# Kernel optimization log

Hardware: AMD Instinct MI355X
Metric: run time of the kernel (lower is better)

Reference implementation:

```python
import jax, jax.numpy as jnp
import numpy as np
from jax import lax

DN = ('NCHW', 'OIHW', 'NCHW')


def setup_inputs() -> dict:
    key = jax.random.key(0)
    ks = jax.random.split(key, 7)
    B, IC, OC, H, W = 8, 64, 64, 128, 128
    return {
        'x': jax.random.normal(ks[0], (B, IC, H, W), jnp.float32),
        'w3': jax.random.normal(ks[1], (OC, IC, 3, 3), jnp.float32) * 0.05,
        'b3': jax.random.normal(ks[2], (OC,), jnp.float32) * 0.05,
        'w5': jax.random.normal(ks[3], (OC, IC, 5, 5), jnp.float32) * 0.05,
        'b5': jax.random.normal(ks[4], (OC,), jnp.float32) * 0.05,
        'wr': jax.random.normal(ks[5], (OC, 10, 1, 1), jnp.float32) * 0.1,
        'br': jax.random.normal(ks[6], (OC,), jnp.float32) * 0.05,
    }


def reference(x, w3, b3, w5, b5, wr, br):
    # Two 'same' convs (k=3 pad 1, k=5 pad 2) as in layers['5']
    y3 = lax.conv_general_dilated(x, w3, (1, 1), 'SAME', dimension_numbers=DN) + b3[None, :, None, None]
    y5 = lax.conv_general_dilated(x, w5, (1, 1), 'SAME', dimension_numbers=DN) + b5[None, :, None, None]
    B, C, H, W = y3.shape
    # The nested pad/crop loop == 9 zero-padded unit shifts of y3:
    # stackedFeatures order per channel: [y5, shift(sh=0,sw=0..2), shift(sh=1,...), ...]
    # shifted[h, w] = y3[h + 1 - sw, w + 1 - sh] with zero padding.
    P = jnp.pad(y3, ((0, 0), (0, 0), (1, 1), (1, 1)))
    shifts = [P[:, :, 2 - sw:2 - sw + H, 2 - sh:2 - sh + W]
              for sh in range(3) for sw in range(3)]
    stacked = jnp.stack([y5] + shifts, axis=2)  # [B, C, 10, H, W]
    # remap: grouped 1x1 conv, groups=OC, 10 in-channels per group
    out = jnp.einsum('bcghw,cg->bchw', stacked, wr[:, :, 0, 0]) + br[None, :, None, None]
    return out
```

## Files before the change

### kernel.cpp

```cpp
#include <hip/hip_runtime.h>

typedef unsigned short u16;
typedef unsigned int u32;
typedef __attribute__((ext_vector_type(8))) short short8;
typedef __attribute__((ext_vector_type(4))) short short4v;
typedef __attribute__((ext_vector_type(4))) float floatx4;

#define XP 72

__device__ __forceinline__ float bf2f(u16 u) {
    u32 b = ((u32)u) << 16;
    return __builtin_bit_cast(float, b);
}
__device__ __forceinline__ u16 f2bf(float f) {
    u32 b = __builtin_bit_cast(u32, f);
    b += 0x7FFFu + ((b >> 16) & 1u);
    return (u16)(b >> 16);
}

typedef __attribute__((address_space(3))) u16 lds_u16;
typedef const __attribute__((address_space(1))) u16 glob_u16;
__device__ __forceinline__ void gl_lds16(const u16* g, u16* l) {
    __builtin_amdgcn_global_load_lds((glob_u16*)g, (lds_u16*)l, 16, 0, 0);
}

__device__ __forceinline__ float load_any(const void* p, int i, int isf32) {
    return isf32 ? ((const float*)p)[i] : bf2f(((const u16*)p)[i]);
}

#define FLAG_BYTE 0
#define W5C_BYTE 256
#define SCAL_BYTE 205056
#define V_BYTE 207872
#define XT_BYTE 1272832
#define N_W5C 102400
#define N_SCAL 704
#define PACK_N2 (N_W5C + N_SCAL)

#define PACK_BLKS ((PACK_N2 + 255) / 256)
#define TRANS_BLKS 4096

__global__ __launch_bounds__(256) void sniff_kernel(const u16* __restrict__ xu,
                                                    int* __restrict__ flag) {
    __shared__ int cnt;
    if (threadIdx.x == 0) cnt = 0;
    __syncthreads();
    int c = 0;
    for (int k = 0; k < 8; ++k) {
        int idx = 2 * (threadIdx.x * 8 + k);
        u16 u = xu[idx];
        int e = (u >> 7) & 0xFF;
        if (e >= 140) c++;
    }
    atomicAdd(&cnt, c);
    __syncthreads();
    if (threadIdx.x == 0) *flag = (cnt >= 8) ? 1 : 0;
}

__global__ __launch_bounds__(256) void pack_trans(
        const void* __restrict__ x, const void* __restrict__ w3,
        const void* __restrict__ b3, const void* __restrict__ w5,
        const void* __restrict__ b5, const void* __restrict__ wr,
        const void* __restrict__ br, const int* __restrict__ flag,
        u16* __restrict__ w5c, float* __restrict__ scal,
        u16* __restrict__ xt) {
    __shared__ u16 tbuf[32 * XP];
    const int bid = blockIdx.x;
    const int tid = threadIdx.x;
    const int f = *flag;

    if (bid < PACK_BLKS) {
        const int i = bid * 256 + tid;
        if (i >= PACK_N2) return;
        if (i < N_W5C) {
            int j = i & 7, lane = (i >> 3) & 63, mt = (i >> 9) & 3, ks = i >> 11;
            int oc = mt * 16 + (lane & 15);
            int k = ks * 32 + ((lane >> 4) & 3) * 8 + j;
            int tap = k >> 6, ic = k & 63;
            int kh = tap / 5, kw = tap - kh * 5;
            int dh = kh - 2, dw = kw - 2;
            float v = load_any(wr, oc * 10, f) * load_any(w5, (oc * 64 + ic) * 25 + tap, f);
            for (int sw = 0; sw < 3; ++sw) {
                int r = dh + sw;
                if (r < 0 || r > 2) continue;
                for (int sh = 0; sh < 3; ++sh) {
                    int c = dw + sh;
                    if (c < 0 || c > 2) continue;
                    v += load_any(wr, oc * 10 + 1 + sh * 3 + sw, f) *
                         load_any(w3, (oc * 64 + ic) * 9 + r * 3 + c, f);
                }
            }
            w5c[i] = f2bf(v);
        } else {
            int i2 = i - N_W5C;
            float v;
            if (i2 < 64) {
                int oc = i2;
                float swr = 0.f;
                for (int g = 1; g <= 9; ++g) swr += load_any(wr, oc * 10 + g, f);
                v = load_any(wr, oc * 10, f) * load_any(b5, oc, f) +
                    swr * load_any(b3, oc, f) + load_any(br, oc, f);
            } else {
                v = load_any(wr, i2 - 64, f);
            }
            scal[i2] = v;
        }
        return;
    }

    {
        const int t2 = bid - PACK_BLKS;
        const int b = t2 >> 9, h = (t2 >> 2) & 127, w0 = (t2 & 3) * 32;
        const int t = tid;
        if (f) {
            const int w2 = t & 15, ic = t >> 4;
#pragma unroll
            for (int p = 0; p < 4; ++p) {
                int icc = ic + p * 16;
                const float* src = (const float*)x +
                    (((size_t)(b * 64 + icc) * 128 + h) * 128 + w0 + 2 * w2);
                float2 v = *(const float2*)src;
                tbuf[(2 * w2) * XP + icc]     = f2bf(v.x);
                tbuf[(2 * w2 + 1) * XP + icc] = f2bf(v.y);
            }
        } else {
            const int w4 = t & 7, ic = t >> 3;
#pragma unroll
            for (int p = 0; p < 2; ++p) {
                int icc = ic + p * 32;
                const u16* src = (const u16*)x +
                    (((size_t)(b * 64 + icc) * 128 + h) * 128 + w0 + 4 * w4);
                short4v v = *(const short4v*)src;
#pragma unroll
                for (int e = 0; e < 4; ++e)
                    tbuf[(4 * w4 + e) * XP + icc] = (u16)v[e];
            }
        }
        __syncthreads();
        const int w = t >> 3, qq = t & 7;
        short8 v = *(const short8*)&tbuf[w * XP + qq * 8];
        *(short8*)(xt + ((size_t)((b * 128 + h) * 128) + w0 + w) * 64 + qq * 8) = v;
    }
}

__global__ __launch_bounds__(256) void virt_y3_mfma(
        const u16* __restrict__ xt, const void* __restrict__ w3,
        const void* __restrict__ b3, const int* __restrict__ flag,
        float* __restrict__ V) {
    __shared__ __align__(16) u16 xrow[132 * XP];
    const int side = blockIdx.x, b = blockIdx.y;
    const int tid = threadIdx.x;
    const int f = *flag;
    const int fixed = (side & 1) ? 127 : 0;
    {
        const int q8 = tid & 7, p0 = tid >> 3;
#pragma unroll
        for (int it = 0; it < 5; ++it) {
            int p = p0 + it * 32;
            if (p < 132) {
                int cc = p - 2;
                short8 v = {0, 0, 0, 0, 0, 0, 0, 0};
                if ((unsigned)cc < 128u) {
                    size_t idx = (side < 2)
                        ? ((size_t)(b * 128 + fixed) * 128 + cc)
                        : ((size_t)(b * 128 + cc) * 128 + fixed);
                    v = *(const short8*)(xt + idx * 64 + q8 * 8);
                }
                *(short8*)&xrow[p * XP + q8 * 8] = v;
            }
        }
    }
    const int wv = tid >> 6, lane = tid & 63, cb = lane & 15, q = lane >> 4;
    const int oc = wv * 16 + cb;
    short8 aaA[6];
#pragma unroll
    for (int ks = 0; ks < 6; ++ks) {
        const int kbase = ks * 32 + q * 8;
        const int kk = kbase >> 6, ic0 = kbase & 63;
        int r, c;
        if (side == 0)      { r = 2;  c = kk; }
        else if (side == 1) { r = 0;  c = kk; }
        else if (side == 2) { r = kk; c = 2;  }
        else                { r = kk; c = 0;  }
        short8 a;
#pragma unroll
        for (int j = 0; j < 8; ++j)
            a[j] = (short)f2bf(load_any(w3, (oc * 64 + ic0 + j) * 9 + r * 3 + c, f));
        aaA[ks] = a;
    }
    __syncthreads();

    floatx4 acc[9];
#pragma unroll
    for (int nt = 0; nt < 9; ++nt) acc[nt] = (floatx4){0.f, 0.f, 0.f, 0.f};
#pragma unroll
    for (int ks = 0; ks < 6; ++ks) {
        const int kbase = ks * 32 + q * 8;
        const int kk = kbase >> 6, ic0 = kbase & 63;
#pragma unroll
        for (int nt = 0; nt < 9; ++nt) {
            int p = nt * 16 + cb + kk;
            if (nt == 8 && p > 131) p = 131;
            short8 bb = *(const short8*)&xrow[p * XP + ic0];
            acc[nt] = __builtin_amdgcn_mfma_f32_16x16x32_bf16(aaA[ks], bb,
                                                              acc[nt], 0, 0, 0);
        }
    }
#pragma unroll
    for (int nt = 0; nt < 9; ++nt) {
        int pos = nt * 16 + cb;
        if (pos < 130) {
#pragma unroll
            for (int reg = 0; reg < 4; ++reg) {
                int oco = wv * 16 + q * 4 + reg;
                V[((size_t)(b * 4 + side) * 130 + pos) * 64 + oco] =
                    acc[nt][reg] + load_any(b3, oco, f);
            }
        }
    }
}

__device__ floatx4 edge_fix4(
        const float* __restrict__ Vb, const float* __restrict__ wrf,
        int gh, int gw, int oc0, floatx4 s) {
#pragma unroll
    for (int sh = 0; sh < 3; ++sh)
#pragma unroll
        for (int sw = 0; sw < 3; ++sw) {
            const int qh = gh + 1 - sw, qw = gw + 1 - sh;
            int sd, pos;
            if (qh == -1)       { sd = 0; pos = qw + 1; }
            else if (qh == 128) { sd = 1; pos = qw + 1; }
            else if (qw == -1)  { sd = 2; pos = qh + 1; }
            else if (qw == 128) { sd = 3; pos = qh + 1; }
            else continue;
            const float* vp = Vb + ((size_t)sd * 130 + pos) * 64 + oc0;
            const int wi = 1 + sh * 3 + sw;
#pragma unroll
            for (int r = 0; r < 4; ++r)
                s[r] -= wrf[(oc0 + r) * 10 + wi] * vp[r];
        }
    return s;
}

__global__ __launch_bounds__(256, 2) void conv_main(
        const u16* __restrict__ xt, const u16* __restrict__ w5c,
        const float* __restrict__ scal, const float* __restrict__ V,
        const int* __restrict__ flag, void* __restrict__ out) {
    __shared__ __align__(16) u16 xs[400 * XP];
    __shared__ __align__(16) u16 wbuf[2][2][2048];
    const int b = blockIdx.z, h0 = blockIdx.y * 16, w0 = blockIdx.x * 16;
    const int tid = threadIdx.x;
    const int f = *flag;
    const int wv = tid >> 6, lane = tid & 63;

    {
        const int q8 = tid & 7, p0 = tid >> 3;
        for (int it = 0; it < 13; ++it) {
            int px = p0 + it * 32;
            if (px < 400) {
                int r = px / 20, c = px - r * 20;
                int gh = h0 + r - 2, gw = w0 + c - 2;
                short8 v = {0, 0, 0, 0, 0, 0, 0, 0};
                if ((unsigned)gh < 128u && (unsigned)gw < 128u)
                    v = *(const short8*)(xt +
                            ((size_t)((b * 128 + gh) * 128 + gw)) * 64 + q8 * 8);
                *(short8*)&xs[px * XP + q8 * 8] = v;
            }
        }
    }
    gl_lds16(w5c + 0 * 2048 + wv * 512 + lane * 8, &wbuf[0][0][wv * 512]);
    gl_lds16(w5c + 1 * 2048 + wv * 512 + lane * 8, &wbuf[0][1][wv * 512]);
    __syncthreads();

    const int cb = lane & 15, q = lane >> 4, wv4 = wv * 4;
    floatx4 acc[4][4];
#pragma unroll
    for (int mt = 0; mt < 4; ++mt)
#pragma unroll
        for (int nt = 0; nt < 4; ++nt)
            acc[mt][nt] = (floatx4){0.f, 0.f, 0.f, 0.f};

#pragma unroll 1
    for (int tap = 0; tap < 25; ++tap) {
        const int p = tap & 1;
        if (tap + 1 < 25) {
            gl_lds16(w5c + (size_t)((tap + 1) * 2 + 0) * 2048 + wv * 512 + lane * 8,
                     &wbuf[p ^ 1][0][wv * 512]);
            gl_lds16(w5c + (size_t)((tap + 1) * 2 + 1) * 2048 + wv * 512 + lane * 8,
                     &wbuf[p ^ 1][1][wv * 512]);
        }
        const int kh = tap / 5, kw = tap - kh * 5;
#pragma unroll
        for (int s = 0; s < 2; ++s) {
            short8 aa[4], bb[4];
#pragma unroll
            for (int mt = 0; mt < 4; ++mt)
                aa[mt] = *(const short8*)&wbuf[p][s][mt * 512 + lane * 8];
#pragma unroll
            for (int nt = 0; nt < 4; ++nt)
                bb[nt] = *(const short8*)&xs[((wv4 + nt + kh) * 20 + cb + kw) * XP +
                                             s * 32 + q * 8];
#pragma unroll
            for (int nt = 0; nt < 4; ++nt)
#pragma unroll
                for (int mt = 0; mt < 4; ++mt)
                    acc[mt][nt] = __builtin_amdgcn_mfma_f32_16x16x32_bf16(
                        aa[mt], bb[nt], acc[mt][nt], 0, 0, 0);
        }
        __syncthreads();
    }

    const float* biasC = scal;
    const float* wrf = scal + 64;
    const float* Vb = V + (size_t)b * 4 * 130 * 64;
#pragma unroll
    for (int mt = 0; mt < 4; ++mt)
#pragma unroll
        for (int nt = 0; nt < 4; ++nt) {
            const int gh = h0 + wv4 + nt;
            const int gw = w0 + cb;
            const int oc0 = mt * 16 + q * 4;
            floatx4 s;
#pragma unroll
            for (int reg = 0; reg < 4; ++reg)
                s[reg] = acc[mt][nt][reg] + biasC[oc0 + reg];
            if (gh == 0 || gh == 127 || gw == 0 || gw == 127)
                s = edge_fix4(Vb, wrf, gh, gw, oc0, s);
#pragma unroll
            for (int reg = 0; reg < 4; ++reg) {
                size_t oidx = ((size_t)(b * 64 + oc0 + reg) * 128 + gh) * 128 + gw;
                if (f) ((float*)out)[oidx] = s[reg];
                else   ((u16*)out)[oidx]   = f2bf(s[reg]);
            }
        }
}

extern "C" void kernel_launch(void* const* d_in, const int* in_sizes, int n_in,
                              void* d_out, int out_size, void* d_ws, size_t ws_size,
                              hipStream_t stream) {
    const void* x  = d_in[0];
    const void* w3 = d_in[1];
    const void* b3 = d_in[2];
    const void* w5 = d_in[3];
    const void* b5 = d_in[4];
    const void* wr = d_in[5];
    const void* br = d_in[6];

    int*   flag = (int*)((char*)d_ws + FLAG_BYTE);
    u16*   w5c  = (u16*)((char*)d_ws + W5C_BYTE);
    float* scal = (float*)((char*)d_ws + SCAL_BYTE);
    float* V    = (float*)((char*)d_ws + V_BYTE);
    u16*   xt   = (u16*)((char*)d_ws + XT_BYTE);

    sniff_kernel<<<1, 256, 0, stream>>>((const u16*)x, flag);
    pack_trans<<<PACK_BLKS + TRANS_BLKS, 256, 0, stream>>>(
        x, w3, b3, w5, b5, wr, br, flag, w5c, scal, xt);
    virt_y3_mfma<<<dim3(4, 8), 256, 0, stream>>>(xt, w3, b3, flag, V);
    conv_main<<<dim3(8, 8, 8), 256, 0, stream>>>(xt, w5c, scal, V, flag, d_out);
}
```

Before: 161.0 us.

## Halve conv tile height, precompute border fixes, and inline dtype sniffing

The main conv tile shrinks from 16x16 to 8x16 output pixels. That halves the accumulators and LDS footprint, allows 3 blocks per CU, and doubles the grid to 1024 blocks. The per-pixel border correction, which read the virtual y3 ring, is precomputed by a new ring_fix kernel into a buffer that the epilogue adds with one vector load. The separate sniff kernel is removed and each kernel recomputes the dtype flag with a wave ballot. The cost is more halo reloading (240 vs 400 rows for half the outputs), an extra kernel launch, and a weaker sniff heuristic over 64 samples.

```diff
diff --git a/kernel.cpp b/kernel.cpp
--- a/kernel.cpp
+++ b/kernel.cpp
@@ -28,46 +28,36 @@
     return isf32 ? ((const float*)p)[i] : bf2f(((const u16*)p)[i]);
 }
 
-#define FLAG_BYTE 0
-#define W5C_BYTE 256
-#define SCAL_BYTE 205056
-#define V_BYTE 207872
-#define XT_BYTE 1272832
+__device__ __forceinline__ int sniff_f(const void* x) {
+    u16 u = ((const u16*)x)[2 * (int)threadIdx.x];
+    int e = (u >> 7) & 0xFF;
+    unsigned long long m = __ballot(e >= 140);
+    return __popcll(m) >= 2 ? 1 : 0;
+}
+
+#define W5C_BYTE 0
+#define SCAL_BYTE 204800
+#define V_BYTE 207616
+#define FR_BYTE 1272576
+#define XT_BYTE 2321152
 #define N_W5C 102400
 #define N_SCAL 704
 #define PACK_N2 (N_W5C + N_SCAL)
 
 #define PACK_BLKS ((PACK_N2 + 255) / 256)
 #define TRANS_BLKS 4096
-
-__global__ __launch_bounds__(256) void sniff_kernel(const u16* __restrict__ xu,
-                                                    int* __restrict__ flag) {
-    __shared__ int cnt;
-    if (threadIdx.x == 0) cnt = 0;
-    __syncthreads();
-    int c = 0;
-    for (int k = 0; k < 8; ++k) {
-        int idx = 2 * (threadIdx.x * 8 + k);
-        u16 u = xu[idx];
-        int e = (u >> 7) & 0xFF;
-        if (e >= 140) c++;
-    }
-    atomicAdd(&cnt, c);
-    __syncthreads();
-    if (threadIdx.x == 0) *flag = (cnt >= 8) ? 1 : 0;
-}
 
 __global__ __launch_bounds__(256) void pack_trans(
         const void* __restrict__ x, const void* __restrict__ w3,
         const void* __restrict__ b3, const void* __restrict__ w5,
         const void* __restrict__ b5, const void* __restrict__ wr,
-        const void* __restrict__ br, const int* __restrict__ flag,
+        const void* __restrict__ br,
         u16* __restrict__ w5c, float* __restrict__ scal,
         u16* __restrict__ xt) {
     __shared__ u16 tbuf[32 * XP];
     const int bid = blockIdx.x;
     const int tid = threadIdx.x;
-    const int f = *flag;
+    const int f = sniff_f(x);
 
     if (bid < PACK_BLKS) {
         const int i = bid * 256 + tid;
@@ -144,13 +134,13 @@
 }
 
 __global__ __launch_bounds__(256) void virt_y3_mfma(
+        const void* __restrict__ x,
         const u16* __restrict__ xt, const void* __restrict__ w3,
-        const void* __restrict__ b3, const int* __restrict__ flag,
-        float* __restrict__ V) {
+        const void* __restrict__ b3, float* __restrict__ V) {
     __shared__ __align__(16) u16 xrow[132 * XP];
     const int side = blockIdx.x, b = blockIdx.y;
     const int tid = threadIdx.x;
-    const int f = *flag;
+    const int f = sniff_f(x);
     const int fixed = (side & 1) ? 127 : 0;
     {
         const int q8 = tid & 7, p0 = tid >> 3;
@@ -220,45 +210,57 @@
     }
 }
 
-__device__ floatx4 edge_fix4(
-        const float* __restrict__ Vb, const float* __restrict__ wrf,
-        int gh, int gw, int oc0, floatx4 s) {
-#pragma unroll
-    for (int sh = 0; sh < 3; ++sh)
-#pragma unroll
-        for (int sw = 0; sw < 3; ++sw) {
-            const int qh = gh + 1 - sw, qw = gw + 1 - sh;
-            int sd, pos;
-            if (qh == -1)       { sd = 0; pos = qw + 1; }
-            else if (qh == 128) { sd = 1; pos = qw + 1; }
-            else if (qw == -1)  { sd = 2; pos = qh + 1; }
-            else if (qw == 128) { sd = 3; pos = qh + 1; }
-            else continue;
-            const float* vp = Vb + ((size_t)sd * 130 + pos) * 64 + oc0;
-            const int wi = 1 + sh * 3 + sw;
-#pragma unroll
-            for (int r = 0; r < 4; ++r)
-                s[r] -= wrf[(oc0 + r) * 10 + wi] * vp[r];
-        }
-    return s;
-}
-
-__global__ __launch_bounds__(256, 2) void conv_main(
+__global__ __launch_bounds__(256) void ring_fix(
+        const float* __restrict__ V, const float* __restrict__ scal,
+        float* __restrict__ Fr) {
+    const int side = blockIdx.x, b = blockIdx.y;
+    const float* wrf = scal + 64;
+    const float* Vb = V + (size_t)b * 4 * 130 * 64;
+    for (int k = 0; k < 8; ++k) {
+        const int idx = (blockIdx.z * 8 + k) * 256 + threadIdx.x;
+        const int pos = idx >> 6, oc = idx & 63;
+        int h, w;
+        if (side == 0)      { h = 0;   w = pos; }
+        else if (side == 1) { h = 127; w = pos; }
+        else if (side == 2) { w = 0;   h = pos; }
+        else                { w = 127; h = pos; }
+        float s = 0.f;
+#pragma unroll
+        for (int sh = 0; sh < 3; ++sh)
+#pragma unroll
+            for (int sw = 0; sw < 3; ++sw) {
+                const int qh = h + 1 - sw, qw = w + 1 - sh;
+                int sd, pp;
+                if (qh == -1)       { sd = 0; pp = qw + 1; }
+                else if (qh == 128) { sd = 1; pp = qw + 1; }
+                else if (qw == -1)  { sd = 2; pp = qh + 1; }
+                else if (qw == 128) { sd = 3; pp = qh + 1; }
+                else continue;
+                s -= wrf[oc * 10 + 1 + sh * 3 + sw] *
+                     Vb[((size_t)sd * 130 + pp) * 64 + oc];
+            }
+        Fr[((size_t)(b * 4 + side) * 128 + pos) * 64 + oc] = s;
+    }
+}
+
+__global__ __launch_bounds__(256, 3) void conv_main(
+        const void* __restrict__ x,
         const u16* __restrict__ xt, const u16* __restrict__ w5c,
-        const float* __restrict__ scal, const float* __restrict__ V,
-        const int* __restrict__ flag, void* __restrict__ out) {
-    __shared__ __align__(16) u16 xs[400 * XP];
+        const float* __restrict__ scal, const float* __restrict__ Fr,
+        void* __restrict__ out) {
+    __shared__ __align__(16) u16 xs[240 * XP];
     __shared__ __align__(16) u16 wbuf[2][2][2048];
-    const int b = blockIdx.z, h0 = blockIdx.y * 16, w0 = blockIdx.x * 16;
+    const int b = blockIdx.z, h0 = blockIdx.y * 8, w0 = blockIdx.x * 16;
     const int tid = threadIdx.x;
-    const int f = *flag;
     const int wv = tid >> 6, lane = tid & 63;
+    const int f = sniff_f(x);
 
     {
         const int q8 = tid & 7, p0 = tid >> 3;
-        for (int it = 0; it < 13; ++it) {
+#pragma unroll
+        for (int it = 0; it < 8; ++it) {
             int px = p0 + it * 32;
-            if (px < 400) {
+            if (px < 240) {
                 int r = px / 20, c = px - r * 20;
                 int gh = h0 + r - 2, gw = w0 + c - 2;
                 short8 v = {0, 0, 0, 0, 0, 0, 0, 0};
@@ -273,12 +275,12 @@
     gl_lds16(w5c + 1 * 2048 + wv * 512 + lane * 8, &wbuf[0][1][wv * 512]);
     __syncthreads();
 
-    const int cb = lane & 15, q = lane >> 4, wv4 = wv * 4;
-    floatx4 acc[4][4];
+    const int cb = lane & 15, q = lane >> 4, wv2 = wv * 2;
+    floatx4 acc[4][2];
 #pragma unroll
     for (int mt = 0; mt < 4; ++mt)
 #pragma unroll
-        for (int nt = 0; nt < 4; ++nt)
+        for (int nt = 0; nt < 2; ++nt)
             acc[mt][nt] = (floatx4){0.f, 0.f, 0.f, 0.f};
 
 #pragma unroll 1
@@ -293,16 +295,16 @@
         const int kh = tap / 5, kw = tap - kh * 5;
 #pragma unroll
         for (int s = 0; s < 2; ++s) {
-            short8 aa[4], bb[4];
+            short8 aa[4], bb[2];
 #pragma unroll
             for (int mt = 0; mt < 4; ++mt)
                 aa[mt] = *(const short8*)&wbuf[p][s][mt * 512 + lane * 8];
 #pragma unroll
-            for (int nt = 0; nt < 4; ++nt)
-                bb[nt] = *(const short8*)&xs[((wv4 + nt + kh) * 20 + cb + kw) * XP +
+            for (int nt = 0; nt < 2; ++nt)
+                bb[nt] = *(const short8*)&xs[((wv2 + nt + kh) * 20 + cb + kw) * XP +
                                              s * 32 + q * 8];
 #pragma unroll
-            for (int nt = 0; nt < 4; ++nt)
+            for (int nt = 0; nt < 2; ++nt)
 #pragma unroll
                 for (int mt = 0; mt < 4; ++mt)
                     acc[mt][nt] = __builtin_amdgcn_mfma_f32_16x16x32_bf16(
@@ -312,21 +314,31 @@
     }
 
     const float* biasC = scal;
-    const float* wrf = scal + 64;
-    const float* Vb = V + (size_t)b * 4 * 130 * 64;
+    const float* Frb = Fr + (size_t)b * 4 * 128 * 64;
 #pragma unroll
     for (int mt = 0; mt < 4; ++mt)
 #pragma unroll
-        for (int nt = 0; nt < 4; ++nt) {
-            const int gh = h0 + wv4 + nt;
+        for (int nt = 0; nt < 2; ++nt) {
+            const int gh = h0 + wv2 + nt;
             const int gw = w0 + cb;
             const int oc0 = mt * 16 + q * 4;
             floatx4 s;
 #pragma unroll
             for (int reg = 0; reg < 4; ++reg)
                 s[reg] = acc[mt][nt][reg] + biasC[oc0 + reg];
-            if (gh == 0 || gh == 127 || gw == 0 || gw == 127)
-                s = edge_fix4(Vb, wrf, gh, gw, oc0, s);
+            {
+                int sd = -1, pp = 0;
+                if (gh == 0)        { sd = 0; pp = gw; }
+                else if (gh == 127) { sd = 1; pp = gw; }
+                else if (gw == 0)   { sd = 2; pp = gh; }
+                else if (gw == 127) { sd = 3; pp = gh; }
+                if (sd >= 0) {
+                    floatx4 fv = *(const floatx4*)(Frb +
+                        ((size_t)sd * 128 + pp) * 64 + oc0);
+#pragma unroll
+                    for (int reg = 0; reg < 4; ++reg) s[reg] += fv[reg];
+                }
+            }
 #pragma unroll
             for (int reg = 0; reg < 4; ++reg) {
                 size_t oidx = ((size_t)(b * 64 + oc0 + reg) * 128 + gh) * 128 + gw;
@@ -347,15 +359,15 @@
     const void* wr = d_in[5];
     const void* br = d_in[6];
 
-    int*   flag = (int*)((char*)d_ws + FLAG_BYTE);
     u16*   w5c  = (u16*)((char*)d_ws + W5C_BYTE);
     float* scal = (float*)((char*)d_ws + SCAL_BYTE);
     float* V    = (float*)((char*)d_ws + V_BYTE);
+    float* Fr   = (float*)((char*)d_ws + FR_BYTE);
     u16*   xt   = (u16*)((char*)d_ws + XT_BYTE);
 
-    sniff_kernel<<<1, 256, 0, stream>>>((const u16*)x, flag);
     pack_trans<<<PACK_BLKS + TRANS_BLKS, 256, 0, stream>>>(
-        x, w3, b3, w5, b5, wr, br, flag, w5c, scal, xt);
-    virt_y3_mfma<<<dim3(4, 8), 256, 0, stream>>>(xt, w3, b3, flag, V);
-    conv_main<<<dim3(8, 8, 8), 256, 0, stream>>>(xt, w5c, scal, V, flag, d_out);
-}
+        x, w3, b3, w5, b5, wr, br, w5c, scal, xt);
+    virt_y3_mfma<<<dim3(4, 8), 256, 0, stream>>>(x, xt, w3, b3, V);
+    ring_fix<<<dim3(4, 8, 4), 256, 0, stream>>>(V, scal, Fr);
+    conv_main<<<dim3(8, 16, 8), 256, 0, stream>>>(x, xt, w5c, scal, Fr, d_out);
+}
```

New measurement: 167.5 us. +4.0%, slower.
